# Kernel tuning notes

Measured on AMD Instinct MI355X. Metric: run time of the kernel, lower is better.

## Reference

```python
import jax, jax.numpy as jnp
import numpy as np

B, S, D, H = 4, 2048, 1024, 16
DK = D // H


def setup_inputs() -> dict:
    key = jax.random.key(0)
    kx, kq, kk, kv, ko = jax.random.split(key, 5)
    scale = D ** -0.5
    return {
        "x": jax.random.normal(kx, (B, S, D), dtype=jnp.float32),
        "W_q": jax.random.normal(kq, (D, D), dtype=jnp.float32) * scale,
        "W_k": jax.random.normal(kk, (D, D), dtype=jnp.float32) * scale,
        "W_v": jax.random.normal(kv, (D, D), dtype=jnp.float32) * scale,
        "W_o": jax.random.normal(ko, (D, D), dtype=jnp.float32) * scale,
    }


def reference(x, W_q, W_k, W_v, W_o):
    b, s, d = x.shape
    # projections: x @ W.T  (weights stored [out, in])
    def proj(W):
        return (x @ W.T).reshape(b, s, H, DK).transpose(0, 2, 1, 3)  # [b,h,s,dk]
    Q, K, V = proj(W_q), proj(W_k), proj(W_v)
    scores = jnp.einsum('bhqd,bhkd->bhqk', Q, K) * (DK ** -0.5)
    causal = jnp.tril(jnp.ones((s, s), dtype=bool))
    scores = jnp.where(causal, scores, -jnp.inf)
    attn = jax.nn.softmax(scores, axis=-1)
    out = jnp.einsum('bhqk,bhkd->bhqd', attn, V)  # [b,h,s,dk]
    out = out.transpose(0, 2, 1, 3).reshape(b, s, d)
    return out @ W_o.T
```

## Files before the change

kernel.cpp:

```cpp
#include <hip/hip_runtime.h>
#include <stdint.h>

#define B_ 4
#define S_ 2048
#define D_ 1024
#define H_ 16
#define DK_ 64
#define M_ (B_*S_)

typedef __attribute__((ext_vector_type(8))) short bhalf8;
typedef __attribute__((ext_vector_type(4))) short bhalf4;
typedef __attribute__((ext_vector_type(4))) float floatx4;
typedef unsigned short bfu;
typedef unsigned int u32;

__device__ __forceinline__ bfu f2bf(float f) {
  union { float f; u32 u; } v; v.f = f;
  u32 r = v.u + 0x7FFFu + ((v.u >> 16) & 1u);
  return (bfu)(r >> 16);
}

__device__ __forceinline__ u32 cvtpk(float a, float b) {
  u32 r;
  asm("v_cvt_pk_bf16_f32 %0, %1, %2" : "=v"(r) : "v"(a), "v"(b));
  return r;
}

__device__ __forceinline__ void gll16(const bfu* g, bfu* l) {
  __builtin_amdgcn_global_load_lds((__attribute__((address_space(1))) void*)g,
                                   (__attribute__((address_space(3))) void*)l,
                                   16, 0, 0);
}

__global__ void cvt_all(const float* __restrict__ x,  const float* __restrict__ wq,
                        const float* __restrict__ wk, const float* __restrict__ wv,
                        const float* __restrict__ wo, bfu* __restrict__ dst) {
  const size_t u = ((size_t)blockIdx.x * blockDim.x + threadIdx.x) * 4;
  const size_t XN = (size_t)M_ * D_;
  const float* src;
  if (u < XN) {
    src = x + u;
  } else {
    const size_t v = u - XN;
    const int wsel = (int)(v >> 20);
    const size_t off = v & ((size_t)(1u << 20) - 1);
    src = ((wsel == 0) ? wq : (wsel == 1) ? wk : (wsel == 2) ? wv : wo) + off;
  }
  float4 vv = *(const float4*)src;
  ushort4 o;
  o.x = f2bf(vv.x); o.y = f2bf(vv.y); o.z = f2bf(vv.z); o.w = f2bf(vv.w);
  *(ushort4*)(dst + u) = o;
}

__device__ __forceinline__ void gemm_core_2ph(const bfu* __restrict__ A,
                                              const bfu* __restrict__ Bw,
                                              bfu* smem,
                                              int m0, int bn0,
                                              floatx4 (&acc)[4][4])
{
  const int tid  = threadIdx.x;
  const int lane = tid & 63;
  const int g    = lane >> 4;
  const int i16  = lane & 15;
  const int w    = tid >> 6;
  const int wm   = w >> 1, wn = w & 1;

  const int lrow = lane >> 3;
  const int scol = ((lane & 7) ^ lrow) << 3;
  const bfu* As = A  + (size_t)(m0  + w * 32 + lrow) * D_ + scol;
  const bfu* Bs = Bw + (size_t)(bn0 + w * 32 + lrow) * D_ + scol;
  const int ldst = w * 4 * 512;

  auto STAGE = [&](int t) {
    bfu* base = smem + (t & 1) * 16384;
    const int k0 = t * 64;
#pragma unroll
    for (int j = 0; j < 4; ++j)
      gll16(As + (size_t)j * 8 * D_ + k0, base + ldst + j * 512);
#pragma unroll
    for (int j = 0; j < 4; ++j)
      gll16(Bs + (size_t)j * 8 * D_ + k0, base + 8192 + ldst + j * 512);
  };

  auto COMPUTE = [&](int t) {
    const char* aTc = (const char*)(smem + (t & 1) * 16384);
    const char* bTc = aTc + 16384;
    __builtin_amdgcn_s_setprio(1);
#pragma unroll
    for (int kb = 0; kb < 2; ++kb) {
      bhalf8 af[4], bf[4];
#pragma unroll
      for (int f = 0; f < 4; ++f) {
        int arow = wm * 64 + f * 16 + i16;
        af[f] = *(const bhalf8*)(aTc + arow * 128 + ((kb * 64 + g * 16) ^ ((arow & 7) << 4)));
        int brow = wn * 64 + f * 16 + i16;
        bf[f] = *(const bhalf8*)(bTc + brow * 128 + ((kb * 64 + g * 16) ^ ((brow & 7) << 4)));
      }
#pragma unroll
      for (int fm = 0; fm < 4; ++fm)
#pragma unroll
        for (int fn = 0; fn < 4; ++fn)
          acc[fm][fn] = __builtin_amdgcn_mfma_f32_16x16x32_bf16(af[fm], bf[fn], acc[fm][fn], 0, 0, 0);
    }
    __builtin_amdgcn_s_setprio(0);
  };

  STAGE(0);
  __syncthreads();
  for (int t = 0; t < 16; ++t) {
    if (t + 1 < 16) STAGE(t + 1);
    COMPUTE(t);
    __syncthreads();
  }
}

__global__ __launch_bounds__(256) void qkv_gemm(const bfu* __restrict__ xb,
                                                const bfu* __restrict__ wqkv,
                                                bfu* __restrict__ Qd,
                                                bfu* __restrict__ Kd,
                                                bfu* __restrict__ Vtd)
{
  __shared__ bfu smem[2 * 16384];
  const int bid = blockIdx.x;
  const int wi   = bid >> 3;
  const int xblk = wi >> 3;
  const int y    = ((bid & 7) << 3) | (wi & 7);
  const int m0   = y * 128;
  const int z    = xblk >> 3;
  const int n0   = (xblk & 7) * 128;
  const int bn0  = xblk * 128;

  floatx4 acc[4][4] = {};
  gemm_core_2ph(xb, wqkv, smem, m0, bn0, acc);

  bfu* dst = (z == 0) ? Qd : (z == 1) ? Kd : Vtd;
  const int lane = threadIdx.x & 63;
  const int g = lane >> 4, i16 = lane & 15;
  const int w = threadIdx.x >> 6, wm = w >> 1, wn = w & 1;
#pragma unroll
  for (int fm = 0; fm < 4; ++fm) {
#pragma unroll
    for (int fn = 0; fn < 4; ++fn) {
      int col = n0 + wn * 64 + fn * 16 + i16;
      int h = col >> 6, dk = col & 63;
#pragma unroll
      for (int r = 0; r < 4; ++r) {
        int mrow = m0 + wm * 64 + fm * 16 + g * 4 + r;
        int b = mrow >> 11, s = mrow & (S_ - 1);
        size_t idx = (z == 2)
            ? ((size_t)((b * H_ + h) * DK_ + dk)) * S_ + s
            : ((size_t)((b * H_ + h) * S_ + s)) * DK_ + dk;
        dst[idx] = f2bf(acc[fm][fn][r]);
      }
    }
  }
}

__global__ __launch_bounds__(256) void out_gemm(const bfu* __restrict__ Ab,
                                                const bfu* __restrict__ wob,
                                                float* __restrict__ out)
{
  __shared__ bfu smem[2 * 16384];
  const int bid = blockIdx.x;
  const int wi   = bid >> 3;
  const int xblk = wi >> 3;
  const int y    = ((bid & 7) << 3) | (wi & 7);
  const int m0   = y * 128;
  const int n0   = xblk * 128;

  floatx4 acc[4][4] = {};
  gemm_core_2ph(Ab, wob, smem, m0, n0, acc);

  const int lane = threadIdx.x & 63;
  const int g = lane >> 4, i16 = lane & 15;
  const int w = threadIdx.x >> 6, wm = w >> 1, wn = w & 1;
#pragma unroll
  for (int fm = 0; fm < 4; ++fm)
#pragma unroll
    for (int fn = 0; fn < 4; ++fn) {
      int col = n0 + wn * 64 + fn * 16 + i16;
#pragma unroll
      for (int r = 0; r < 4; ++r) {
        int mrow = m0 + wm * 64 + fm * 16 + g * 4 + r;
        out[(size_t)mrow * D_ + col] = acc[fm][fn][r];
      }
    }
}

template<int BUF>
__device__ __forceinline__ void attn_tile(const char* smem, int t, int ntw, int qr,
                                          int koff0, int koff1, const int (&voff)[4],
                                          bhalf8 qa0, bhalf8 qa1, int g, int i16,
                                          floatx4 (&ot)[4], float& mC2, float& lp)
{
  const float C2 = 0.125f * 1.44269504f;
  floatx4 sa[4] = {};
#pragma unroll
  for (int cb = 0; cb < 4; ++cb) {
    bhalf8 kf0 = *(const bhalf8*)(smem + BUF + cb * 2048 + koff0);
    bhalf8 kf1 = *(const bhalf8*)(smem + BUF + cb * 2048 + koff1);
    sa[cb] = __builtin_amdgcn_mfma_f32_16x16x32_bf16(kf0, qa0, sa[cb], 0, 0, 0);
    sa[cb] = __builtin_amdgcn_mfma_f32_16x16x32_bf16(kf1, qa1, sa[cb], 0, 0, 0);
  }
  if (t == ntw - 1) {
    const int kv0 = t * 64;
#pragma unroll
    for (int cb = 0; cb < 4; ++cb)
#pragma unroll
      for (int r = 0; r < 4; ++r)
        if (kv0 + cb * 16 + g * 4 + r > qr + i16) sa[cb][r] = -3.0e38f;
  }
  float pm = sa[0][0];
#pragma unroll
  for (int cb = 0; cb < 4; ++cb)
#pragma unroll
    for (int r = 0; r < 4; ++r)
      pm = fmaxf(pm, sa[cb][r]);
  pm = fmaxf(pm, __shfl_xor(pm, 16));
  pm = fmaxf(pm, __shfl_xor(pm, 32));
  const float pmC2 = pm * C2;
  if (!__all(pmC2 - mC2 <= 8.0f)) {
    const float nmax = fmaxf(mC2, pmC2);
    const float al = exp2f(mC2 - nmax);
    mC2 = nmax;
    lp *= al;
#pragma unroll
    for (int da = 0; da < 4; ++da)
#pragma unroll
      for (int r = 0; r < 4; ++r)
        ot[da][r] *= al;
  }
  const float nm = -mC2;
  u32 pk[8];
  float ps = 0.f;
#pragma unroll
  for (int cb = 0; cb < 4; ++cb) {
    float p0 = exp2f(__builtin_fmaf(sa[cb][0], C2, nm));
    float p1 = exp2f(__builtin_fmaf(sa[cb][1], C2, nm));
    float p2 = exp2f(__builtin_fmaf(sa[cb][2], C2, nm));
    float p3 = exp2f(__builtin_fmaf(sa[cb][3], C2, nm));
    ps += (p0 + p1) + (p2 + p3);
    pk[cb * 2]     = cvtpk(p0, p1);
    pk[cb * 2 + 1] = cvtpk(p2, p3);
  }
  lp += ps;
#pragma unroll
  for (int da = 0; da < 4; ++da) {
#pragma unroll
    for (int cb = 0; cb < 4; ++cb) {
      bhalf4 vf = *(const bhalf4*)(smem + BUF + voff[cb] + da * 2048);
      union { u32 u[2]; bhalf4 h; } pu;
      pu.u[0] = pk[cb * 2]; pu.u[1] = pk[cb * 2 + 1];
      ot[da] = __builtin_amdgcn_mfma_f32_16x16x16bf16_1k(vf, pu.h, ot[da], 0, 0, 0);
    }
  }
}

__global__ __launch_bounds__(512, 4) void attn_kernel(const bfu* __restrict__ Q,
                                                      const bfu* __restrict__ Kc,
                                                      const bfu* __restrict__ Vt,
                                                      bfu* __restrict__ Oc)
{
  __shared__ char smem[32768];
  const int tid = threadIdx.x;
  const int lane = tid & 63;
  const int w = tid >> 6;
  const int g = lane >> 4, i16 = lane & 15;
  const int sw = (i16 & 7) << 4;
  const int bh = blockIdx.x;
  const int y  = 15 - blockIdx.y;

  const bfu* Qb = Q  + (size_t)bh * S_ * DK_;
  const bfu* Kb = Kc + (size_t)bh * S_ * DK_;
  const bfu* Vb = Vt + (size_t)bh * DK_ * S_;
  const int b = bh >> 4, h = bh & 15;

  const int srow = tid >> 3;
  const int scolb = (tid & 7) * 16;
  const bfu* kgp = Kb + srow * DK_ + (scolb >> 1);
  const bfu* vgp = Vb + (size_t)srow * S_ + (scolb >> 1);
  char* kld = smem + srow * 128 + (scolb ^ ((srow & 7) << 4));
  const int vsw = ((srow & 7) << 4) | (srow & 8);
  char* vld0 = smem + 8192 + srow * 128 + ((scolb    ) ^ vsw);
  char* vld1 = smem + 8192 + srow * 128 + ((scolb + 8) ^ vsw);

  const int koff0 = i16 * 128 + ((g * 16) ^ sw);
  const int koff1 = i16 * 128 + ((64 + g * 16) ^ sw);
  const int vswr = sw | (i16 & 8);
  int voff[4];
#pragma unroll
  for (int cb = 0; cb < 4; ++cb)
    voff[cb] = 8192 + i16 * 128 + ((cb * 32 + g * 8) ^ vswr);

  const int ntw = 2 * y + 1 + (w >> 2);
  const int qr = y * 128 + w * 16;
  const int npair = y + 1;

  bhalf8 qa0 = *(const bhalf8*)(Qb + (size_t)(qr + i16) * DK_ + g * 8);
  bhalf8 qa1 = *(const bhalf8*)(Qb + (size_t)(qr + i16) * DK_ + 32 + g * 8);

  floatx4 ot[4] = {};
  float mC2 = -1.0e30f;
  float lp  = 0.f;

  union { bhalf8 h8; bhalf4 h4[2]; } vu;
  bhalf8 ka, va, kb2, vb2;
  ka  = *(const bhalf8*)kgp;                  va  = *(const bhalf8*)vgp;
  kb2 = *(const bhalf8*)(kgp + 4096);         vb2 = *(const bhalf8*)(vgp + 64);
  *(bhalf8*)kld = ka;  vu.h8 = va;  *(bhalf4*)vld0 = vu.h4[0]; *(bhalf4*)vld1 = vu.h4[1];
  *(bhalf8*)(kld + 16384) = kb2; vu.h8 = vb2;
  *(bhalf4*)(vld0 + 16384) = vu.h4[0]; *(bhalf4*)(vld1 + 16384) = vu.h4[1];
  __syncthreads();

  for (int p = 0; ; ++p) {
    const bool more = (p + 1 < npair);
    if (more) {
      ka  = *(const bhalf8*)(kgp + (size_t)(2 * p + 2) * 4096);
      va  = *(const bhalf8*)(vgp + (2 * p + 2) * 64);
      kb2 = *(const bhalf8*)(kgp + (size_t)(2 * p + 3) * 4096);
      vb2 = *(const bhalf8*)(vgp + (2 * p + 3) * 64);
    }
    const int t0 = 2 * p;
    attn_tile<0>(smem, t0, ntw, qr, koff0, koff1, voff, qa0, qa1, g, i16, ot, mC2, lp);
    if (t0 + 1 < ntw)
      attn_tile<16384>(smem, t0 + 1, ntw, qr, koff0, koff1, voff, qa0, qa1, g, i16, ot, mC2, lp);
    if (!more) break;
    __syncthreads();
    *(bhalf8*)kld = ka;  vu.h8 = va;
    *(bhalf4*)vld0 = vu.h4[0]; *(bhalf4*)vld1 = vu.h4[1];
    *(bhalf8*)(kld + 16384) = kb2; vu.h8 = vb2;
    *(bhalf4*)(vld0 + 16384) = vu.h4[0]; *(bhalf4*)(vld1 + 16384) = vu.h4[1];
    __syncthreads();
  }

  float lt = lp;
  lt += __shfl_xor(lt, 16);
  lt += __shfl_xor(lt, 32);
  const float rl = 1.0f / lt;
  const size_t rowbase = (size_t)(b * S_ + qr + i16) * D_ + h * 64;
#pragma unroll
  for (int da = 0; da < 4; ++da) {
    union { u32 u[2]; uint2 v; } ov;
    ov.u[0] = cvtpk(ot[da][0] * rl, ot[da][1] * rl);
    ov.u[1] = cvtpk(ot[da][2] * rl, ot[da][3] * rl);
    *(uint2*)(Oc + rowbase + da * 16 + g * 4) = ov.v;
  }
}

extern "C" void kernel_launch(void* const* d_in, const int* in_sizes, int n_in,
                              void* d_out, int out_size, void* d_ws, size_t ws_size,
                              hipStream_t stream)
{
  const float* x  = (const float*)d_in[0];
  const float* wq = (const float*)d_in[1];
  const float* wk = (const float*)d_in[2];
  const float* wv = (const float*)d_in[3];
  const float* wo = (const float*)d_in[4];

  bfu* xb  = (bfu*)d_ws;
  bfu* wqb = xb  + (size_t)M_ * D_;
  bfu* wob = wqb + (size_t)3 * D_ * D_;
  bfu* Qd  = wob + (size_t)D_ * D_;
  bfu* Kd  = Qd  + (size_t)M_ * D_;
  bfu* Vtd = Kd  + (size_t)M_ * D_;
  bfu* Ad  = Vtd + (size_t)M_ * D_;

  const size_t total = (size_t)M_ * D_ + 4 * (size_t)D_ * D_;
  cvt_all<<<(int)(total / 4 / 256), 256, 0, stream>>>(x, wq, wk, wv, wo, xb);

  qkv_gemm<<<1536, 256, 0, stream>>>(xb, wqb, Qd, Kd, Vtd);
  attn_kernel<<<dim3(B_ * H_, 16), 512, 0, stream>>>(Qd, Kd, Vtd, Ad);
  out_gemm<<<512, 256, 0, stream>>>(Ad, wob, (float*)d_out);
}
```

Baseline: 185.0 us.

## Process two 16-row query subtiles per wave in attention to double K/V reuse

Each wave now handles 32 query rows (two 16-row subtiles), so every K and V fragment read from shared memory feeds two MFMAs. Each block covers 256 query rows instead of 128, and the grid is halved to 8 blocks per head. This cuts LDS traffic and the number of K/V tile loads per query, at the cost of more registers (doubled accumulators and softmax state), fewer blocks, and coarser causal load balance.

```diff
diff --git a/kernel.cpp b/kernel.cpp
--- a/kernel.cpp
+++ b/kernel.cpp
@@ -188,70 +188,81 @@
 }
 
 template<int BUF>
-__device__ __forceinline__ void attn_tile(const char* smem, int t, int ntw, int qr,
-                                          int koff0, int koff1, const int (&voff)[4],
-                                          bhalf8 qa0, bhalf8 qa1, int g, int i16,
-                                          floatx4 (&ot)[4], float& mC2, float& lp)
+__device__ __forceinline__ void attn_tile2(const char* smem, int t, int ntw, int qr,
+                                           int koff0, int koff1, const int (&voff)[4],
+                                           const bhalf8 (&qa)[2][2], int g, int i16,
+                                           floatx4 (&ot)[2][4], float (&mC2)[2], float (&lp)[2])
 {
   const float C2 = 0.125f * 1.44269504f;
-  floatx4 sa[4] = {};
+  floatx4 sa[2][4] = {};
 #pragma unroll
   for (int cb = 0; cb < 4; ++cb) {
     bhalf8 kf0 = *(const bhalf8*)(smem + BUF + cb * 2048 + koff0);
     bhalf8 kf1 = *(const bhalf8*)(smem + BUF + cb * 2048 + koff1);
-    sa[cb] = __builtin_amdgcn_mfma_f32_16x16x32_bf16(kf0, qa0, sa[cb], 0, 0, 0);
-    sa[cb] = __builtin_amdgcn_mfma_f32_16x16x32_bf16(kf1, qa1, sa[cb], 0, 0, 0);
+    sa[0][cb] = __builtin_amdgcn_mfma_f32_16x16x32_bf16(kf0, qa[0][0], sa[0][cb], 0, 0, 0);
+    sa[0][cb] = __builtin_amdgcn_mfma_f32_16x16x32_bf16(kf1, qa[0][1], sa[0][cb], 0, 0, 0);
+    sa[1][cb] = __builtin_amdgcn_mfma_f32_16x16x32_bf16(kf0, qa[1][0], sa[1][cb], 0, 0, 0);
+    sa[1][cb] = __builtin_amdgcn_mfma_f32_16x16x32_bf16(kf1, qa[1][1], sa[1][cb], 0, 0, 0);
   }
   if (t == ntw - 1) {
     const int kv0 = t * 64;
 #pragma unroll
+    for (int qs = 0; qs < 2; ++qs) {
+      const int q = qr + qs * 16 + i16;
+#pragma unroll
+      for (int cb = 0; cb < 4; ++cb)
+#pragma unroll
+        for (int r = 0; r < 4; ++r)
+          if (kv0 + cb * 16 + g * 4 + r > q) sa[qs][cb][r] = -3.0e38f;
+    }
+  }
+  u32 pk[2][8];
+#pragma unroll
+  for (int qs = 0; qs < 2; ++qs) {
+    float pm = sa[qs][0][0];
+#pragma unroll
     for (int cb = 0; cb < 4; ++cb)
 #pragma unroll
       for (int r = 0; r < 4; ++r)
-        if (kv0 + cb * 16 + g * 4 + r > qr + i16) sa[cb][r] = -3.0e38f;
-  }
-  float pm = sa[0][0];
-#pragma unroll
-  for (int cb = 0; cb < 4; ++cb)
-#pragma unroll
-    for (int r = 0; r < 4; ++r)
-      pm = fmaxf(pm, sa[cb][r]);
-  pm = fmaxf(pm, __shfl_xor(pm, 16));
-  pm = fmaxf(pm, __shfl_xor(pm, 32));
-  const float pmC2 = pm * C2;
-  if (!__all(pmC2 - mC2 <= 8.0f)) {
-    const float nmax = fmaxf(mC2, pmC2);
-    const float al = exp2f(mC2 - nmax);
-    mC2 = nmax;
-    lp *= al;
-#pragma unroll
-    for (int da = 0; da < 4; ++da)
-#pragma unroll
-      for (int r = 0; r < 4; ++r)
-        ot[da][r] *= al;
-  }
-  const float nm = -mC2;
-  u32 pk[8];
-  float ps = 0.f;
-#pragma unroll
-  for (int cb = 0; cb < 4; ++cb) {
-    float p0 = exp2f(__builtin_fmaf(sa[cb][0], C2, nm));
-    float p1 = exp2f(__builtin_fmaf(sa[cb][1], C2, nm));
-    float p2 = exp2f(__builtin_fmaf(sa[cb][2], C2, nm));
-    float p3 = exp2f(__builtin_fmaf(sa[cb][3], C2, nm));
-    ps += (p0 + p1) + (p2 + p3);
-    pk[cb * 2]     = cvtpk(p0, p1);
-    pk[cb * 2 + 1] = cvtpk(p2, p3);
-  }
-  lp += ps;
+        pm = fmaxf(pm, sa[qs][cb][r]);
+    pm = fmaxf(pm, __shfl_xor(pm, 16));
+    pm = fmaxf(pm, __shfl_xor(pm, 32));
+    const float pmC2 = pm * C2;
+    if (!__all(pmC2 - mC2[qs] <= 8.0f)) {
+      const float nmax = fmaxf(mC2[qs], pmC2);
+      const float al = exp2f(mC2[qs] - nmax);
+      mC2[qs] = nmax;
+      lp[qs] *= al;
+#pragma unroll
+      for (int da = 0; da < 4; ++da)
+#pragma unroll
+        for (int r = 0; r < 4; ++r)
+          ot[qs][da][r] *= al;
+    }
+    const float nm = -mC2[qs];
+    float ps = 0.f;
+#pragma unroll
+    for (int cb = 0; cb < 4; ++cb) {
+      float p0 = exp2f(__builtin_fmaf(sa[qs][cb][0], C2, nm));
+      float p1 = exp2f(__builtin_fmaf(sa[qs][cb][1], C2, nm));
+      float p2 = exp2f(__builtin_fmaf(sa[qs][cb][2], C2, nm));
+      float p3 = exp2f(__builtin_fmaf(sa[qs][cb][3], C2, nm));
+      ps += (p0 + p1) + (p2 + p3);
+      pk[qs][cb * 2]     = cvtpk(p0, p1);
+      pk[qs][cb * 2 + 1] = cvtpk(p2, p3);
+    }
+    lp[qs] += ps;
+  }
 #pragma unroll
   for (int da = 0; da < 4; ++da) {
 #pragma unroll
     for (int cb = 0; cb < 4; ++cb) {
       bhalf4 vf = *(const bhalf4*)(smem + BUF + voff[cb] + da * 2048);
-      union { u32 u[2]; bhalf4 h; } pu;
-      pu.u[0] = pk[cb * 2]; pu.u[1] = pk[cb * 2 + 1];
-      ot[da] = __builtin_amdgcn_mfma_f32_16x16x16bf16_1k(vf, pu.h, ot[da], 0, 0, 0);
+      union { u32 u[2]; bhalf4 h; } p0, p1;
+      p0.u[0] = pk[0][cb * 2]; p0.u[1] = pk[0][cb * 2 + 1];
+      p1.u[0] = pk[1][cb * 2]; p1.u[1] = pk[1][cb * 2 + 1];
+      ot[0][da] = __builtin_amdgcn_mfma_f32_16x16x16bf16_1k(vf, p0.h, ot[0][da], 0, 0, 0);
+      ot[1][da] = __builtin_amdgcn_mfma_f32_16x16x16bf16_1k(vf, p1.h, ot[1][da], 0, 0, 0);
     }
   }
 }
@@ -268,7 +279,7 @@
   const int g = lane >> 4, i16 = lane & 15;
   const int sw = (i16 & 7) << 4;
   const int bh = blockIdx.x;
-  const int y  = 15 - blockIdx.y;
+  const int y  = 7 - blockIdx.y;
 
   const bfu* Qb = Q  + (size_t)bh * S_ * DK_;
   const bfu* Kb = Kc + (size_t)bh * S_ * DK_;
@@ -292,16 +303,20 @@
   for (int cb = 0; cb < 4; ++cb)
     voff[cb] = 8192 + i16 * 128 + ((cb * 32 + g * 8) ^ vswr);
 
-  const int ntw = 2 * y + 1 + (w >> 2);
-  const int qr = y * 128 + w * 16;
-  const int npair = y + 1;
-
-  bhalf8 qa0 = *(const bhalf8*)(Qb + (size_t)(qr + i16) * DK_ + g * 8);
-  bhalf8 qa1 = *(const bhalf8*)(Qb + (size_t)(qr + i16) * DK_ + 32 + g * 8);
-
-  floatx4 ot[4] = {};
-  float mC2 = -1.0e30f;
-  float lp  = 0.f;
+  const int qr = y * 256 + w * 32;
+  const int ntw = (qr >> 6) + 1;
+  const int npair = 2 * y + 2;
+
+  bhalf8 qa[2][2];
+#pragma unroll
+  for (int qs = 0; qs < 2; ++qs)
+#pragma unroll
+    for (int kb = 0; kb < 2; ++kb)
+      qa[qs][kb] = *(const bhalf8*)(Qb + (size_t)(qr + qs * 16 + i16) * DK_ + kb * 32 + g * 8);
+
+  floatx4 ot[2][4] = {};
+  float mC2[2] = { -1.0e30f, -1.0e30f };
+  float lp[2]  = { 0.f, 0.f };
 
   union { bhalf8 h8; bhalf4 h4[2]; } vu;
   bhalf8 ka, va, kb2, vb2;
@@ -321,9 +336,10 @@
       vb2 = *(const bhalf8*)(vgp + (2 * p + 3) * 64);
     }
     const int t0 = 2 * p;
-    attn_tile<0>(smem, t0, ntw, qr, koff0, koff1, voff, qa0, qa1, g, i16, ot, mC2, lp);
+    if (t0 < ntw)
+      attn_tile2<0>(smem, t0, ntw, qr, koff0, koff1, voff, qa, g, i16, ot, mC2, lp);
     if (t0 + 1 < ntw)
-      attn_tile<16384>(smem, t0 + 1, ntw, qr, koff0, koff1, voff, qa0, qa1, g, i16, ot, mC2, lp);
+      attn_tile2<16384>(smem, t0 + 1, ntw, qr, koff0, koff1, voff, qa, g, i16, ot, mC2, lp);
     if (!more) break;
     __syncthreads();
     *(bhalf8*)kld = ka;  vu.h8 = va;
@@ -333,17 +349,20 @@
     __syncthreads();
   }
 
-  float lt = lp;
-  lt += __shfl_xor(lt, 16);
-  lt += __shfl_xor(lt, 32);
-  const float rl = 1.0f / lt;
-  const size_t rowbase = (size_t)(b * S_ + qr + i16) * D_ + h * 64;
-#pragma unroll
-  for (int da = 0; da < 4; ++da) {
-    union { u32 u[2]; uint2 v; } ov;
-    ov.u[0] = cvtpk(ot[da][0] * rl, ot[da][1] * rl);
-    ov.u[1] = cvtpk(ot[da][2] * rl, ot[da][3] * rl);
-    *(uint2*)(Oc + rowbase + da * 16 + g * 4) = ov.v;
+#pragma unroll
+  for (int qs = 0; qs < 2; ++qs) {
+    float lt = lp[qs];
+    lt += __shfl_xor(lt, 16);
+    lt += __shfl_xor(lt, 32);
+    const float rl = 1.0f / lt;
+    const size_t rowbase = (size_t)(b * S_ + qr + qs * 16 + i16) * D_ + h * 64;
+#pragma unroll
+    for (int da = 0; da < 4; ++da) {
+      union { u32 u[2]; uint2 v; } ov;
+      ov.u[0] = cvtpk(ot[qs][da][0] * rl, ot[qs][da][1] * rl);
+      ov.u[1] = cvtpk(ot[qs][da][2] * rl, ot[qs][da][3] * rl);
+      *(uint2*)(Oc + rowbase + da * 16 + g * 4) = ov.v;
+    }
   }
 }
 
@@ -369,6 +388,6 @@
   cvt_all<<<(int)(total / 4 / 256), 256, 0, stream>>>(x, wq, wk, wv, wo, xb);
 
   qkv_gemm<<<1536, 256, 0, stream>>>(xb, wqb, Qd, Kd, Vtd);
-  attn_kernel<<<dim3(B_ * H_, 16), 512, 0, stream>>>(Qd, Kd, Vtd, Ad);
+  attn_kernel<<<dim3(B_ * H_, 8), 512, 0, stream>>>(Qd, Kd, Vtd, Ad);
   out_gemm<<<512, 256, 0, stream>>>(Ad, wob, (float*)d_out);
 }
```

New measurement: 207.2 us. 12.0% more time.
